# Kernel optimization log

Measured on AMD Instinct MI355X. Metric: run time of the kernel, lower is better.

## Reference

```python
import jax, jax.numpy as jnp
import numpy as np

LST = 64  # sparsemax frame length over time


def sparsemax(z):
    """Sparsemax over the last axis (Martins & Astudillo 2016)."""
    d = z.shape[-1]
    z_sorted = jnp.flip(jnp.sort(z, axis=-1), axis=-1)           # descending
    z_cumsum = jnp.cumsum(z_sorted, axis=-1)
    k = jnp.arange(1, d + 1, dtype=z.dtype)
    support = (1.0 + k * z_sorted) > z_cumsum                    # bool, [..., d]
    k_z = jnp.sum(support, axis=-1, keepdims=True)               # int, >=1
    tau_sum = jnp.take_along_axis(z_cumsum, k_z - 1, axis=-1)
    tau = (tau_sum - 1.0) / k_z.astype(z.dtype)
    return jnp.maximum(z - tau, 0.0)


def setup_inputs() -> dict:
    key = jax.random.key(0)
    midis_out = jax.random.normal(key, (16, 11, 65536), dtype=jnp.float32)
    return {"midis_out": midis_out}


def reference(midis_out):
    batch, n_insts, time = midis_out.shape
    lst = LST
    len_pad = (lst - time % lst) % lst
    x = jnp.pad(midis_out, ((0, 0), (0, 0), (0, len_pad)))
    t_pad = time + len_pad
    # sparsemax over instruments: (b, t, i) -> sparsemax over i -> back to (b, i, t)
    out_inst = jnp.swapaxes(sparsemax(jnp.swapaxes(x, 1, 2)), 1, 2)
    # sparsemax over fixed time blocks of length lst
    out_time = sparsemax(x.reshape(batch, n_insts, t_pad // lst, lst))
    out_time = out_time.reshape(batch, n_insts, t_pad)
    return out_inst[:, :, :time] * out_time[:, :, :time]
```

## Files before the change

kernel.cpp:

```cpp
#include <hip/hip_runtime.h>

#define B_   16
#define NI   11
#define T_   65536
#define LST  64
#define NBLK (T_ / LST)
#define ROWP 68

#define DPP_XOR1 0xB1
#define DPP_XOR2 0x4E

__device__ __forceinline__ float frcp(float x) { return __builtin_amdgcn_rcpf(x); }

template<int CTRL>
__device__ __forceinline__ float dppf(float x) {
    return __int_as_float(__builtin_amdgcn_update_dpp(
        0, __float_as_int(x), CTRL, 0xF, 0xF, true));
}
template<int CTRL>
__device__ __forceinline__ int dppi(int x) {
    return __builtin_amdgcn_update_dpp(0, x, CTRL, 0xF, 0xF, true);
}

__global__ __launch_bounds__(256) void fused_sparsemax_kernel(
        const float* __restrict__ in, float* __restrict__ out) {
    __shared__ float ldsz[4][NI * ROWP];
    __shared__ float ldsti[4][64];

    const int lane = threadIdx.x & 63;
    const int wid  = threadIdx.x >> 6;
    const int tile = blockIdx.x * 4 + wid;
    const int b    = tile >> 10;
    const int jb   = tile & (NBLK - 1);

    const float* px = in + (size_t)b * NI * T_ + (size_t)jb * LST + (size_t)lane;

    float z[NI];
#pragma unroll
    for (int i = 0; i < NI; ++i) z[i] = px[(size_t)i * T_];

#pragma unroll
    for (int i = 0; i < NI; ++i) ldsz[wid][i * ROWP + lane] = z[i];

    float mx = z[0];
#pragma unroll
    for (int i = 1; i < NI; ++i) mx = fmaxf(mx, z[i]);
    float tau_i = mx - 1.0f;
    int prevc = 0;
    for (int it = 0; it < NI + 1; ++it) {
        float s = 0.0f;
        int   c = 0;
#pragma unroll
        for (int i = 0; i < NI; ++i) {
            bool a = z[i] > tau_i;
            s += a ? z[i] : 0.0f;
            c += a ? 1 : 0;
        }
        if (!__any(c != prevc)) break;
        prevc = c;
        tau_i = (s - 1.0f) * frcp((float)c);
    }
    ldsti[wid][lane] = tau_i;

    const int g   = lane >> 2;
    const int q   = lane & 3;
    const int row = (g < NI) ? g : (g - NI);

    float y[16];
#pragma unroll
    for (int r = 0; r < 16; ++r) y[r] = ldsz[wid][row * ROWP + q * 16 + r];

    float m = y[0];
#pragma unroll
    for (int r = 1; r < 16; ++r) m = fmaxf(m, y[r]);
    m = fmaxf(m, dppf<DPP_XOR1>(m));
    m = fmaxf(m, dppf<DPP_XOR2>(m));

    float tau = m - 1.0f;
    int prev = 0;
    for (int it = 0; it < LST + 1; ++it) {
        float s = 0.0f;
        int   c = 0;
#pragma unroll
        for (int r = 0; r < 16; ++r) {
            bool a = y[r] > tau;
            s += a ? y[r] : 0.0f;
            c += a ? 1 : 0;
        }
        s += dppf<DPP_XOR1>(s);
        s += dppf<DPP_XOR2>(s);
        c += dppi<DPP_XOR1>(c);
        c += dppi<DPP_XOR2>(c);
        if (!__any(c != prev)) break;
        prev = c;
        tau = (s - 1.0f) * frcp((float)c);
    }

    if (g < NI) {
        float ti[16];
#pragma unroll
        for (int r = 0; r < 16; ++r) ti[r] = ldsti[wid][q * 16 + r];

        float* po = out + (size_t)b * NI * T_ + (size_t)g * T_
                        + (size_t)jb * LST + (size_t)q * 16;
        float4* po4 = reinterpret_cast<float4*>(po);
#pragma unroll
        for (int v = 0; v < 4; ++v) {
            float4 o;
            o.x = fmaxf(y[4*v+0] - tau, 0.0f) * fmaxf(y[4*v+0] - ti[4*v+0], 0.0f);
            o.y = fmaxf(y[4*v+1] - tau, 0.0f) * fmaxf(y[4*v+1] - ti[4*v+1], 0.0f);
            o.z = fmaxf(y[4*v+2] - tau, 0.0f) * fmaxf(y[4*v+2] - ti[4*v+2], 0.0f);
            o.w = fmaxf(y[4*v+3] - tau, 0.0f) * fmaxf(y[4*v+3] - ti[4*v+3], 0.0f);
            po4[v] = o;
        }
    }
}

extern "C" void kernel_launch(void* const* d_in, const int* in_sizes, int n_in,
                              void* d_out, int out_size, void* d_ws, size_t ws_size,
                              hipStream_t stream) {
    const float* in = (const float*)d_in[0];
    float* out = (float*)d_out;
    hipLaunchKernelGGL(fused_sparsemax_kernel, dim3(4096), dim3(256), 0, stream,
                       in, out);
}
```

Measured before the change: 28.51 us.

## Sort instrument axis with odd-even network, unroll early tau iterations, nontemporal stores

Replaces the iterative fixed-point search for the instrument-axis threshold with an 11-element odd-even transposition sort followed by the exact cumsum support test, which removes the data-dependent loop and its wave votes. The time-axis threshold search now runs three unrolled iterations before any convergence check, and skips the sum reduction on the final exiting iteration. Output stores use nontemporal hints. The sort adds a fixed cost of about 55 min/max pairs per lane, and the unconditional iterations may be wasted work when the search converges early.

```diff
diff --git a/kernel.cpp b/kernel.cpp
--- a/kernel.cpp
+++ b/kernel.cpp
@@ -10,6 +10,8 @@
 #define DPP_XOR1 0xB1
 #define DPP_XOR2 0x4E
 
+typedef float f32x4 __attribute__((ext_vector_type(4)));
+
 __device__ __forceinline__ float frcp(float x) { return __builtin_amdgcn_rcpf(x); }
 
 template<int CTRL>
@@ -20,6 +22,12 @@
 template<int CTRL>
 __device__ __forceinline__ int dppi(int x) {
     return __builtin_amdgcn_update_dpp(0, x, CTRL, 0xF, 0xF, true);
+}
+
+__device__ __forceinline__ void ce_desc(float& a, float& b) {
+    float mx = fmaxf(a, b);
+    float mn = fminf(a, b);
+    a = mx; b = mn;
 }
 
 __global__ __launch_bounds__(256) void fused_sparsemax_kernel(
@@ -42,26 +50,6 @@
 #pragma unroll
     for (int i = 0; i < NI; ++i) ldsz[wid][i * ROWP + lane] = z[i];
 
-    float mx = z[0];
-#pragma unroll
-    for (int i = 1; i < NI; ++i) mx = fmaxf(mx, z[i]);
-    float tau_i = mx - 1.0f;
-    int prevc = 0;
-    for (int it = 0; it < NI + 1; ++it) {
-        float s = 0.0f;
-        int   c = 0;
-#pragma unroll
-        for (int i = 0; i < NI; ++i) {
-            bool a = z[i] > tau_i;
-            s += a ? z[i] : 0.0f;
-            c += a ? 1 : 0;
-        }
-        if (!__any(c != prevc)) break;
-        prevc = c;
-        tau_i = (s - 1.0f) * frcp((float)c);
-    }
-    ldsti[wid][lane] = tau_i;
-
     const int g   = lane >> 2;
     const int q   = lane & 3;
     const int row = (g < NI) ? g : (g - NI);
@@ -70,30 +58,67 @@
 #pragma unroll
     for (int r = 0; r < 16; ++r) y[r] = ldsz[wid][row * ROWP + q * 16 + r];
 
+    float s[NI];
+#pragma unroll
+    for (int i = 0; i < NI; ++i) s[i] = z[i];
+#pragma unroll
+    for (int p = 0; p < NI; ++p) {
+#pragma unroll
+        for (int k = (p & 1); k + 1 < NI; k += 2) ce_desc(s[k], s[k + 1]);
+    }
+    float cum = 0.0f, tsum = 0.0f;
+    int   kz  = 0;
+#pragma unroll
+    for (int k = 1; k <= NI; ++k) {
+        cum += s[k - 1];
+        bool cond = fmaf((float)k, s[k - 1], 1.0f) > cum;
+        kz   += cond ? 1 : 0;
+        tsum += cond ? s[k - 1] : 0.0f;
+    }
+    const float tau_i = (tsum - 1.0f) * frcp((float)kz);
+    ldsti[wid][lane] = tau_i;
+
     float m = y[0];
 #pragma unroll
     for (int r = 1; r < 16; ++r) m = fmaxf(m, y[r]);
     m = fmaxf(m, dppf<DPP_XOR1>(m));
     m = fmaxf(m, dppf<DPP_XOR2>(m));
 
-    float tau = m - 1.0f;
-    int prev = 0;
-    for (int it = 0; it < LST + 1; ++it) {
-        float s = 0.0f;
-        int   c = 0;
+    float tau  = m - 1.0f;
+    int   prev = 0;
+#pragma unroll
+    for (int it = 0; it < 3; ++it) {
+        float ss = 0.0f;
+        int   cc = 0;
 #pragma unroll
         for (int r = 0; r < 16; ++r) {
             bool a = y[r] > tau;
-            s += a ? y[r] : 0.0f;
-            c += a ? 1 : 0;
+            ss += a ? y[r] : 0.0f;
+            cc += a ? 1 : 0;
         }
-        s += dppf<DPP_XOR1>(s);
-        s += dppf<DPP_XOR2>(s);
-        c += dppi<DPP_XOR1>(c);
-        c += dppi<DPP_XOR2>(c);
-        if (!__any(c != prev)) break;
-        prev = c;
-        tau = (s - 1.0f) * frcp((float)c);
+        ss += dppf<DPP_XOR1>(ss);
+        ss += dppf<DPP_XOR2>(ss);
+        cc += dppi<DPP_XOR1>(cc);
+        cc += dppi<DPP_XOR2>(cc);
+        tau  = (ss - 1.0f) * frcp((float)cc);
+        prev = cc;
+    }
+    for (int it = 0; it < LST; ++it) {
+        float ss = 0.0f;
+        int   cc = 0;
+#pragma unroll
+        for (int r = 0; r < 16; ++r) {
+            bool a = y[r] > tau;
+            ss += a ? y[r] : 0.0f;
+            cc += a ? 1 : 0;
+        }
+        cc += dppi<DPP_XOR1>(cc);
+        cc += dppi<DPP_XOR2>(cc);
+        if (!__any(cc != prev)) break;
+        ss += dppf<DPP_XOR1>(ss);
+        ss += dppf<DPP_XOR2>(ss);
+        prev = cc;
+        tau  = (ss - 1.0f) * frcp((float)cc);
     }
 
     if (g < NI) {
@@ -103,15 +128,15 @@
 
         float* po = out + (size_t)b * NI * T_ + (size_t)g * T_
                         + (size_t)jb * LST + (size_t)q * 16;
-        float4* po4 = reinterpret_cast<float4*>(po);
+        f32x4* po4 = reinterpret_cast<f32x4*>(po);
 #pragma unroll
         for (int v = 0; v < 4; ++v) {
-            float4 o;
+            f32x4 o;
             o.x = fmaxf(y[4*v+0] - tau, 0.0f) * fmaxf(y[4*v+0] - ti[4*v+0], 0.0f);
             o.y = fmaxf(y[4*v+1] - tau, 0.0f) * fmaxf(y[4*v+1] - ti[4*v+1], 0.0f);
             o.z = fmaxf(y[4*v+2] - tau, 0.0f) * fmaxf(y[4*v+2] - ti[4*v+2], 0.0f);
             o.w = fmaxf(y[4*v+3] - tau, 0.0f) * fmaxf(y[4*v+3] - ti[4*v+3], 0.0f);
-            po4[v] = o;
+            __builtin_nontemporal_store(o, &po4[v]);
         }
     }
 }
```

After: 65.54 us. 2.3x slower.
